# Kernel tuning notes

Hardware: AMD Instinct MI355X
Metric: run time of the kernel (lower is better)

Reference implementation:

```python
import jax, jax.numpy as jnp
import numpy as np

D_MODEL = 2048
N_HEADS = 16
N_KV_HEADS = 4
HEAD_DIM = D_MODEL // N_HEADS  # 128
N_REP = N_HEADS // N_KV_HEADS  # 4
WINDOW = 1024
NUM_META = 128
ROPE_BASE = 10000.0
EPS = 1e-6


def _rmsnorm(x, w):
    # x: [..., HEAD_DIM]; computed in fp32 like the torch module
    xf = x.astype(jnp.float32)
    rms = jax.lax.rsqrt(jnp.mean(xf * xf, axis=-1, keepdims=True) + EPS)
    return (w * xf * rms).astype(x.dtype)


def _apply_rope(x, pos):
    # x: [B, H, T, HEAD_DIM], pos: [B, T] (int) -> interleaved rotary
    inv_freq = 1.0 / (ROPE_BASE ** (jnp.arange(0, HEAD_DIM, 2, dtype=jnp.float32) / HEAD_DIM))  # [HEAD_DIM/2]
    freqs = pos.astype(jnp.float32)[..., None] * inv_freq  # [B, T, HEAD_DIM/2]
    cos = jnp.cos(freqs)[:, None, :, :]  # [B, 1, T, HEAD_DIM/2]
    sin = jnp.sin(freqs)[:, None, :, :]
    x1 = x[..., ::2]
    x2 = x[..., 1::2]
    rot = jnp.stack([x1 * cos - x2 * sin, x1 * sin + x2 * cos], axis=-1)  # [B,H,T,HEAD_DIM/2,2]
    return rot.reshape(x.shape)


def setup_inputs() -> dict:
    key = jax.random.key(0)
    kh, kq, kk, kv, ko = jax.random.split(key, 5)
    B, T = 2, 2048
    s = 0.02
    return {
        'hidden_states': jax.random.normal(kh, (B, T, D_MODEL), dtype=jnp.float32),
        'position_ids': jnp.arange(T, dtype=jnp.int32),
        'Wq': jax.random.normal(kq, (D_MODEL, N_HEADS * HEAD_DIM), dtype=jnp.float32) * s,
        'Wk': jax.random.normal(kk, (D_MODEL, N_KV_HEADS * HEAD_DIM), dtype=jnp.float32) * s,
        'Wv': jax.random.normal(kv, (D_MODEL, N_KV_HEADS * HEAD_DIM), dtype=jnp.float32) * s,
        'Wo': jax.random.normal(ko, (N_HEADS * HEAD_DIM, D_MODEL), dtype=jnp.float32) * s,
        'q_norm_w': jnp.ones((HEAD_DIM,), dtype=jnp.float32),
        'k_norm_w': jnp.ones((HEAD_DIM,), dtype=jnp.float32),
    }


def reference(hidden_states, position_ids, Wq, Wk, Wv, Wo, q_norm_w, k_norm_w):
    B, T, _ = hidden_states.shape
    Tk = T  # no kv_cache / shared_kv in this config

    # QKV projections -> [B, H, T, hd]
    q = (hidden_states @ Wq).reshape(B, T, N_HEADS, HEAD_DIM).transpose(0, 2, 1, 3)
    k = (hidden_states @ Wk).reshape(B, T, N_KV_HEADS, HEAD_DIM).transpose(0, 2, 1, 3)
    v = (hidden_states @ Wv).reshape(B, T, N_KV_HEADS, HEAD_DIM).transpose(0, 2, 1, 3)

    # per-head RMSNorm (before RoPE, as in the torch module)
    q = _rmsnorm(q, q_norm_w)
    k = _rmsnorm(k, k_norm_w)

    # RoPE: queries use position_ids, keys use arange(Tk)
    pos_q = jnp.broadcast_to(position_ids[None, :], (B, T))
    pos_k = jnp.broadcast_to(jnp.arange(Tk)[None, :], (B, Tk))
    q = _apply_rope(q, pos_q)
    k = _apply_rope(k, pos_k)

    # GQA: repeat KV heads (head h uses kv head h // N_REP)
    k = jnp.repeat(k, N_REP, axis=1)
    v = jnp.repeat(v, N_REP, axis=1)

    scale = 1.0 / np.sqrt(HEAD_DIM)
    scores = jnp.einsum('bhqd,bhkd->bhqk', q, k) * scale  # [B,H,T,Tk]

    # sliding-window + meta-token causal mask (offset = Tk - T = 0 here)
    q_idx = jnp.arange(T)[:, None]
    k_idx = jnp.arange(Tk)[None, :]
    win_start = jnp.maximum(q_idx - WINDOW + 1, NUM_META)
    allowed = (k_idx < NUM_META) | ((k_idx >= win_start) & (k_idx <= q_idx))
    scores = jnp.where(allowed[None, None], scores, -jnp.inf)

    probs = jax.nn.softmax(scores, axis=-1)
    out = jnp.einsum('bhqk,bhkd->bhqd', probs, v)  # [B,H,T,hd]
    out = out.transpose(0, 2, 1, 3).reshape(B, T, N_HEADS * HEAD_DIM)
    return out @ Wo
```

## Files before the change

kernel.cpp:

```cpp
#include <hip/hip_runtime.h>
#include <cstdint>
#include <cstddef>

#define DM 2048
#define TT 2048
#define BB 2
#define HQ 16
#define HKV 4
#define HD 128

typedef _Float16 f16;
using f16x8 = __attribute__((ext_vector_type(8))) f16;
using f32x4 = __attribute__((ext_vector_type(4))) float;
using f32x16 = __attribute__((ext_vector_type(16))) float;
using u32x4 = __attribute__((ext_vector_type(4))) uint32_t;

#define MFMA16(a, b, c) __builtin_amdgcn_mfma_f32_16x16x32_f16(a, b, c, 0, 0, 0)
#define MFMA32(a, b, c) __builtin_amdgcn_mfma_f32_32x32x16_f16(a, b, c, 0, 0, 0)

typedef __attribute__((address_space(1))) const void gvoid_t;
typedef __attribute__((address_space(3))) void lvoid_t;
static __device__ __forceinline__ void gload16(const void* g, void* l) {
  __builtin_amdgcn_global_load_lds((gvoid_t*)g, (lvoid_t*)l, 16, 0, 0);
}

static __device__ __forceinline__ float fast_exp2(float x) {
#if __has_builtin(__builtin_amdgcn_exp2f)
  return __builtin_amdgcn_exp2f(x);
#else
  return exp2f(x);
#endif
}

static __device__ __forceinline__ uint32_t cvt_pk_u32(float a, float b) {
  auto h2 = __builtin_amdgcn_cvt_pkrtz(a, b);
  return __builtin_bit_cast(uint32_t, h2);
}

__global__ __launch_bounds__(256) void k_cvt_f16(const float* __restrict__ in,
                                                 f16* __restrict__ out, int n8) {
  int i = blockIdx.x * 256 + threadIdx.x;
  if (i >= n8) return;
  const float4* pin = (const float4*)in;
  float4 a = pin[2 * i], b = pin[2 * i + 1];
  f16x8 o = {(f16)a.x, (f16)a.y, (f16)a.z, (f16)a.w,
             (f16)b.x, (f16)b.y, (f16)b.z, (f16)b.w};
  *(f16x8*)&out[(size_t)8 * i] = o;
}

__global__ __launch_bounds__(256) void k_tr_cvt(const float* __restrict__ in,
                                                f16* __restrict__ out, int N, int ldout) {
  __shared__ float tile[32][33];
  int n0 = blockIdx.x * 32, k0 = blockIdx.y * 32;
  int tx = threadIdx.x, ty = threadIdx.y;
#pragma unroll
  for (int r = 0; r < 32; r += 8) tile[ty + r][tx] = in[(size_t)(k0 + ty + r) * N + n0 + tx];
  __syncthreads();
#pragma unroll
  for (int r = 0; r < 32; r += 8)
    out[(size_t)(n0 + ty + r) * ldout + k0 + tx] = (f16)tile[tx][ty + r];
}

template <int BN_, int N_, bool OUT_F16>
__global__ __launch_bounds__(512, 2) void k_gemm8(const f16* __restrict__ A,
                                                  const f16* __restrict__ BT,
                                                  void* __restrict__ Cp, int M, int K) {
  constexpr int NF = BN_ / 64;
  constexpr int BI = BN_ / 64;
  __shared__ alignas(16) char Abuf[2][256 * 128];
  __shared__ alignas(16) char Bbuf[2][BN_ * 128];
  constexpr int NT = N_ / BN_;
  int bid = blockIdx.x;
  int m0 = (bid / NT) * 256, n0 = (bid % NT) * BN_;
  int tid = threadIdx.x;
  int lane = tid & 63, w = tid >> 6;
  int wr = w >> 2, wc = w & 3;
  int g = lane >> 4, c = lane & 15;
  int rswz = (c & 7) << 4;

  int srow = tid >> 3;
  int scbs = ((tid & 7) * 16) ^ ((srow & 7) << 4);
  const char* Ag = (const char*)A + (size_t)(m0 + srow) * (K * 2) + scbs;
  const char* Bg = (const char*)BT + (size_t)(n0 + srow) * (K * 2) + scbs;
  int lbase = w * 1024;

  f32x4 acc[8][NF] = {};
  int nk = K >> 6;

  auto stageA = [&](int buf, int kt, int i) {
    gload16(Ag + (size_t)(i * 64) * (K * 2) + (size_t)kt * 128,
            &Abuf[buf][i * 8192 + lbase]);
  };
  auto stageB = [&](int buf, int kt, int i) {
    gload16(Bg + (size_t)(i * 64) * (K * 2) + (size_t)kt * 128,
            &Bbuf[buf][i * 8192 + lbase]);
  };

  {
#pragma unroll
    for (int i = 0; i < 4; i++) stageA(0, 0, i);
#pragma unroll
    for (int i = 0; i < BI; i++) stageB(0, 0, i);
    asm volatile("s_waitcnt vmcnt(0)" ::: "memory");
    __builtin_amdgcn_s_barrier();
  }

  for (int kt = 0; kt < nk; kt++) {
    int cur = kt & 1, nxt = cur ^ 1;
    bool more = (kt + 1) < nk;
    const char* Ab = Abuf[cur];
    const char* Bb = Bbuf[cur];
    f16x8 bf[NF][2], af[2][2];
#pragma unroll
    for (int p = 0; p < 4; p++) {
      if (p == 0) {
#pragma unroll
        for (int nn = 0; nn < NF; nn++)
#pragma unroll
          for (int kk = 0; kk < 2; kk++) {
            int R = wc * (NF * 16) + nn * 16 + c;
            bf[nn][kk] = *(const f16x8*)(Bb + R * 128 + ((kk * 64 + g * 16) ^ rswz));
          }
      }
#pragma unroll
      for (int j = 0; j < 2; j++)
#pragma unroll
        for (int kk = 0; kk < 2; kk++) {
          int R = wr * 128 + (p * 2 + j) * 16 + c;
          af[j][kk] = *(const f16x8*)(Ab + R * 128 + ((kk * 64 + g * 16) ^ rswz));
        }
      if (more) {
        if (p == 0) {
          stageA(nxt, kt + 1, 0); stageA(nxt, kt + 1, 1); stageB(nxt, kt + 1, 0);
        } else if (p == 1) {
          stageA(nxt, kt + 1, 2); stageA(nxt, kt + 1, 3); stageB(nxt, kt + 1, 1);
          if constexpr (BI == 3) stageB(nxt, kt + 1, 2);
        }
      }
      __builtin_amdgcn_s_barrier();
      __builtin_amdgcn_s_setprio(1);
#pragma unroll
      for (int j = 0; j < 2; j++)
#pragma unroll
        for (int nn = 0; nn < NF; nn++)
#pragma unroll
          for (int kk = 0; kk < 2; kk++)
            acc[p * 2 + j][nn] = MFMA16(af[j][kk], bf[nn][kk], acc[p * 2 + j][nn]);
      __builtin_amdgcn_s_setprio(0);
    }
    asm volatile("s_waitcnt vmcnt(0)" ::: "memory");
    __builtin_amdgcn_s_barrier();
  }
#pragma unroll
  for (int mm = 0; mm < 8; mm++)
#pragma unroll
    for (int nn = 0; nn < NF; nn++)
#pragma unroll
      for (int r = 0; r < 4; r++) {
        size_t row = m0 + wr * 128 + mm * 16 + g * 4 + r;
        size_t col = n0 + wc * (NF * 16) + nn * 16 + c;
        float v = acc[mm][nn][r];
        if constexpr (OUT_F16)
          ((f16*)Cp)[row * N_ + col] = (f16)v;
        else
          ((float*)Cp)[row * N_ + col] = v;
      }
}

__global__ __launch_bounds__(256) void k_norm_rope(const f16* __restrict__ qkv,
                                                   const int* __restrict__ pos_ids,
                                                   const float* __restrict__ qw,
                                                   const float* __restrict__ kw,
                                                   f16* __restrict__ Qo, f16* __restrict__ Ko) {
  int bt = blockIdx.x;
  int b = bt >> 11, t = bt & 2047;
  int tid = threadIdx.x, w = tid >> 6, lane = tid & 63;
  const f16* row = qkv + (size_t)bt * 3072;
  float pq = (float)pos_ids[t];
  float pk = (float)t;
  float inv = expf(-(float)lane * 0.14391156831212787f);
  float aq = pq * inv, ak = pk * inv;
  float snq = sinf(aq), csq = cosf(aq);
  float snk = sinf(ak), csk = cosf(ak);
  for (int hi = w; hi < 20; hi += 4) {
    bool isq = hi < 16;
    int off = isq ? hi * 128 : 2048 + (hi - 16) * 128;
    float x1 = (float)row[off + 2 * lane];
    float x2 = (float)row[off + 2 * lane + 1];
    float ss = x1 * x1 + x2 * x2;
#pragma unroll
    for (int o = 1; o < 64; o <<= 1) ss += __shfl_xor(ss, o);
    float rms = rsqrtf(ss * (1.0f / 128.0f) + 1e-6f);
    const float* wt = isq ? qw : kw;
    float n1 = x1 * rms * wt[2 * lane], n2 = x2 * rms * wt[2 * lane + 1];
    float sn = isq ? snq : snk, cs = isq ? csq : csk;
    f16 r1 = (f16)(n1 * cs - n2 * sn), r2 = (f16)(n1 * sn + n2 * cs);
    if (isq) {
      f16* dst = Qo + (((size_t)b * HQ + hi) * TT + t) * HD;
      dst[2 * lane] = r1;
      dst[2 * lane + 1] = r2;
    } else {
      f16* dst = Ko + (((size_t)b * HKV + (hi - 16)) * TT + t) * HD;
      dst[2 * lane] = r1;
      dst[2 * lane + 1] = r2;
    }
  }
}

__global__ __launch_bounds__(256) void k_trV(const f16* __restrict__ qkv,
                                             f16* __restrict__ Vt) {
  __shared__ f16 tile[32][34];
  int t0 = blockIdx.x * 32, d0 = blockIdx.y * 32;
  int bh = blockIdx.z;
  int b = bh >> 2, hkv = bh & 3;
  int tx = threadIdx.x, ty = threadIdx.y;
  const f16* src = qkv + (size_t)b * 2048 * 3072 + 2560 + hkv * 128;
#pragma unroll
  for (int r = 0; r < 32; r += 8)
    tile[ty + r][tx] = src[(size_t)(t0 + ty + r) * 3072 + d0 + tx];
  __syncthreads();
  f16* dst = Vt + ((size_t)bh * HD + d0) * TT + t0;
#pragma unroll
  for (int r = 0; r < 32; r += 8)
    dst[(size_t)(ty + r) * TT + tx] = tile[tx][ty + r];
}

__global__ __launch_bounds__(256, 2) void k_attn2(const f16* __restrict__ Q,
                                                  const f16* __restrict__ Kc,
                                                  const f16* __restrict__ Vt,
                                                  f16* __restrict__ Oa) {
  __shared__ alignas(16) char KsC[2][64 * 256];
  __shared__ alignas(16) char VsC[2][128 * 128];
  int qt = blockIdx.x, h = blockIdx.y, b = blockIdx.z;
  qt = b ? (15 - qt) : qt;
  int q0 = qt * 128, hkv = h >> 2;
  int tid = threadIdx.x;
  int w = tid >> 6, lane = tid & 63, ln = lane & 31, hi = lane >> 5;
  const char* KbB = (const char*)(Kc + ((size_t)b * HKV + hkv) * TT * HD);
  const char* VbB = (const char*)(Vt + ((size_t)b * HKV + hkv) * (size_t)HD * TT);
  int q = q0 + w * 32 + ln;
  const f16* Qp = Q + (((size_t)b * HQ + h) * TT + q) * HD + hi * 8;
  f16x8 qf[8];
#pragma unroll
  for (int st = 0; st < 8; st++) qf[st] = *(const f16x8*)&Qp[st * 16];
  f32x16 o[4] = {};
  float lsum = 0.f;
  int kfswz = (ln & 7) << 4;

  int krow0 = w * 4 + (lane >> 4);
  int kswzb = ((lane & 15) * 16) ^ ((krow0 & 7) << 4);
  int vrow0 = w * 8 + (lane >> 3);
  int vswzb = ((lane & 7) * 16) ^ ((vrow0 & 7) << 4);

  int k0max = (q0 + 127) & ~63;
  int wlo = (q0 - 1023 > 128) ? ((q0 - 1023) & ~63) : 128;
  int nw = (k0max >= wlo) ? ((k0max - wlo) >> 6) + 1 : 0;
  int ntiles = 2 + nw;
  int qw = q0 + w * 32;

  const float C1 = 0.12751791217100872f;
  const float C2 = 5.7707801635534255f;

  auto stage = [&](int buf, int k0) {
    const char* ks = KbB + (size_t)(k0 + krow0) * 256 + kswzb;
    const char* vs = VbB + (size_t)vrow0 * (TT * 2) + (size_t)k0 * 2 + vswzb;
    char* kd = KsC[buf] + w * 1024;
    char* vd = VsC[buf] + w * 1024;
#pragma unroll
    for (int j = 0; j < 4; j++) gload16(ks + (size_t)j * 4096, kd + j * 4096);
#pragma unroll
    for (int j = 0; j < 4; j++) gload16(vs + (size_t)j * 32 * (TT * 2), vd + j * 4096);
  };

  stage(0, 0);
  __syncthreads();
  int cur = 0;

  for (int ti = 0; ti < ntiles; ti++) {
    int k0 = (ti < 2) ? ti * 64 : wlo + (ti - 2) * 64;
    bool havenext = (ti + 1 < ntiles);
    if (havenext) {
      int k0n = (ti + 1 < 2) ? 64 : wlo + (ti - 1) * 64;
      stage(cur ^ 1, k0n);
    }
    bool needmask = false;
    if (ti >= 2) {
      int wsmax = qw + 31 - 1023;
      if (wsmax < 128) wsmax = 128;
      needmask = !((k0 + 63 <= qw) && (k0 >= wsmax));
    }
    f16x8 pa[2][2];
#pragma unroll
    for (int ksub = 0; ksub < 2; ksub++) {
      f32x16 s0 = {}, s1 = {};
      const char* krow = KsC[cur] + (ksub * 32 + ln) * 256;
      __builtin_amdgcn_s_setprio(1);
#pragma unroll
      for (int st = 0; st < 8; st += 2) {
        f16x8 kf0 = *(const f16x8*)(krow + ((st * 32 + hi * 16) ^ kfswz));
        f16x8 kf1 = *(const f16x8*)(krow + (((st + 1) * 32 + hi * 16) ^ kfswz));
        s0 = MFMA32(kf0, qf[st], s0);
        s1 = MFMA32(kf1, qf[st + 1], s1);
      }
      __builtin_amdgcn_s_setprio(0);
      f32x16 s = s0 + s1;
      int qmk = q - (k0 + ksub * 32 + 4 * hi);
      float pr[16];
#pragma unroll
      for (int r = 0; r < 16; r++) {
        float e = fast_exp2(s[r] * C1 - C2);
        if (needmask) {
          int kk = (r & 3) + 8 * (r >> 2);
          e = ((uint32_t)(qmk - kk) < 1024u) ? e : 0.0f;
        }
        lsum += e;
        pr[r] = e;
      }
      uint32_t c[8];
#pragma unroll
      for (int i = 0; i < 8; i++) c[i] = cvt_pk_u32(pr[2 * i], pr[2 * i + 1]);
      {
        uint32_t x0 = __shfl_xor(c[0], 32), x1 = __shfl_xor(c[1], 32);
        uint32_t x2 = __shfl_xor(c[2], 32), x3 = __shfl_xor(c[3], 32);
        u32x4 t0 = {hi ? x2 : c[0], hi ? x3 : c[1], hi ? c[2] : x0, hi ? c[3] : x1};
        pa[ksub][0] = __builtin_bit_cast(f16x8, t0);
        uint32_t x4 = __shfl_xor(c[4], 32), x5 = __shfl_xor(c[5], 32);
        uint32_t x6 = __shfl_xor(c[6], 32), x7 = __shfl_xor(c[7], 32);
        u32x4 t1 = {hi ? x6 : c[4], hi ? x7 : c[5], hi ? c[6] : x4, hi ? c[7] : x5};
        pa[ksub][1] = __builtin_bit_cast(f16x8, t1);
      }
    }
    __builtin_amdgcn_s_setprio(1);
#pragma unroll
    for (int dsub = 0; dsub < 4; dsub++) {
      const char* vrow = VsC[cur] + (dsub * 32 + ln) * 128;
#pragma unroll
      for (int ksub = 0; ksub < 2; ksub++)
#pragma unroll
        for (int st2 = 0; st2 < 2; st2++) {
          f16x8 vf = *(const f16x8*)(vrow + ((ksub * 64 + st2 * 32 + hi * 16) ^ kfswz));
          o[dsub] = MFMA32(pa[ksub][st2], vf, o[dsub]);
        }
    }
    __builtin_amdgcn_s_setprio(0);
    __syncthreads();
    cur ^= 1;
  }
  lsum += __shfl_xor(lsum, 32);
  float rl[16];
#pragma unroll
  for (int r = 0; r < 16; r++) {
    int row = (r & 3) + 8 * (r >> 2) + 4 * hi;
    float lv = __shfl(lsum, row);
    rl[r] = 1.0f / lv;
  }
#pragma unroll
  for (int r = 0; r < 16; r++) {
    int row = (r & 3) + 8 * (r >> 2) + 4 * hi;
    size_t base = ((size_t)b * TT + q0 + w * 32 + row) * DM + (size_t)h * HD + ln;
#pragma unroll
    for (int dsub = 0; dsub < 4; dsub++)
      Oa[base + dsub * 32] = (f16)(o[dsub][r] * rl[r]);
  }
}

extern "C" void kernel_launch(void* const* d_in, const int* in_sizes, int n_in,
                              void* d_out, int out_size, void* d_ws, size_t ws_size,
                              hipStream_t stream) {
  const float* hidden = (const float*)d_in[0];
  const int* pos = (const int*)d_in[1];
  const float* Wq = (const float*)d_in[2];
  const float* Wk = (const float*)d_in[3];
  const float* Wv = (const float*)d_in[4];
  const float* Wo = (const float*)d_in[5];
  const float* qw = (const float*)d_in[6];
  const float* kw = (const float*)d_in[7];
  float* out = (float*)d_out;

  char* p = (char*)d_ws;
  auto take = [&](size_t n) {
    void* r = (void*)p;
    p += (n + 255) & ~(size_t)255;
    return r;
  };
  f16* Xb = (f16*)take((size_t)4096 * 2048 * 2);
  f16* WqkvT = (f16*)take((size_t)3072 * 2048 * 2);
  f16* WoT = (f16*)take((size_t)2048 * 2048 * 2);
  f16* QKVb = (f16*)take((size_t)4096 * 3072 * 2);
  f16* Qr = (f16*)take((size_t)BB * HQ * TT * HD * 2);
  f16* Kr = (f16*)take((size_t)BB * HKV * TT * HD * 2);
  f16* Vt = (f16*)take((size_t)BB * HKV * TT * HD * 2);
  f16* Attn = (f16*)take((size_t)4096 * 2048 * 2);

  dim3 tb(32, 8);
  k_cvt_f16<<<4096, 256, 0, stream>>>(hidden, Xb, 1048576);
  k_tr_cvt<<<dim3(64, 64), tb, 0, stream>>>(Wq, WqkvT, 2048, 2048);
  k_tr_cvt<<<dim3(16, 64), tb, 0, stream>>>(Wk, WqkvT + (size_t)2048 * 2048, 512, 2048);
  k_tr_cvt<<<dim3(16, 64), tb, 0, stream>>>(Wv, WqkvT + (size_t)2560 * 2048, 512, 2048);
  k_tr_cvt<<<dim3(64, 64), tb, 0, stream>>>(Wo, WoT, 2048, 2048);
  k_gemm8<192, 3072, true><<<256, 512, 0, stream>>>(Xb, WqkvT, QKVb, 4096, 2048);
  k_norm_rope<<<4096, 256, 0, stream>>>(QKVb, pos, qw, kw, Qr, Kr);
  k_trV<<<dim3(64, 4, 8), tb, 0, stream>>>(QKVb, Vt);
  k_attn2<<<dim3(16, 16, 2), 256, 0, stream>>>(Qr, Kr, Vt, Attn);
  k_gemm8<128, 2048, false><<<256, 512, 0, stream>>>(Attn, WoT, out, 4096, 2048);
}
```

Baseline: 199.9 us.

## Merge weight transposes into one launch, remap GEMM blocks and attention q-tiles

Combines the four weight transpose/convert launches into a single kernel that dispatches on block index, cutting launch overhead and the tail gaps between launches. The GEMM block index is permuted with a stride-8 remap, probably to spread tiles sharing A/B rows across XCDs or L2 for better cache locality. Attention q-tile ordering now interleaves short and long causal tiles within each batch, to balance load across concurrently scheduled blocks. Each remap changes which CUs get which work and could lower cache reuse if the assumed block scheduling does not hold.

```diff
diff --git a/kernel.cpp b/kernel.cpp
--- a/kernel.cpp
+++ b/kernel.cpp
@@ -48,17 +48,34 @@
   *(f16x8*)&out[(size_t)8 * i] = o;
 }
 
-__global__ __launch_bounds__(256) void k_tr_cvt(const float* __restrict__ in,
-                                                f16* __restrict__ out, int N, int ldout) {
+__global__ __launch_bounds__(256) void k_tr_all(const float* __restrict__ Wq,
+                                                const float* __restrict__ Wk,
+                                                const float* __restrict__ Wv,
+                                                const float* __restrict__ Wo,
+                                                f16* __restrict__ WqkvT,
+                                                f16* __restrict__ WoT) {
   __shared__ float tile[32][33];
-  int n0 = blockIdx.x * 32, k0 = blockIdx.y * 32;
+  int t = blockIdx.x;
+  const float* in;
+  f16* out;
+  int N, nx;
+  if (t < 4096) {
+    in = Wq; out = WqkvT; N = 2048; nx = 64;
+  } else if (t < 5120) {
+    t -= 4096; in = Wk; out = WqkvT + (size_t)2048 * 2048; N = 512; nx = 16;
+  } else if (t < 6144) {
+    t -= 5120; in = Wv; out = WqkvT + (size_t)2560 * 2048; N = 512; nx = 16;
+  } else {
+    t -= 6144; in = Wo; out = WoT; N = 2048; nx = 64;
+  }
+  int n0 = (t % nx) * 32, k0 = (t / nx) * 32;
   int tx = threadIdx.x, ty = threadIdx.y;
 #pragma unroll
   for (int r = 0; r < 32; r += 8) tile[ty + r][tx] = in[(size_t)(k0 + ty + r) * N + n0 + tx];
   __syncthreads();
 #pragma unroll
   for (int r = 0; r < 32; r += 8)
-    out[(size_t)(n0 + ty + r) * ldout + k0 + tx] = (f16)tile[tx][ty + r];
+    out[(size_t)(n0 + ty + r) * 2048 + k0 + tx] = (f16)tile[tx][ty + r];
 }
 
 template <int BN_, int N_, bool OUT_F16>
@@ -70,7 +87,8 @@
   __shared__ alignas(16) char Abuf[2][256 * 128];
   __shared__ alignas(16) char Bbuf[2][BN_ * 128];
   constexpr int NT = N_ / BN_;
-  int bid = blockIdx.x;
+  int bid0 = blockIdx.x;
+  int bid = (bid0 & 7) * (gridDim.x >> 3) + (bid0 >> 3);
   int m0 = (bid / NT) * 256, n0 = (bid % NT) * BN_;
   int tid = threadIdx.x;
   int lane = tid & 63, w = tid >> 6;
@@ -232,7 +250,7 @@
   __shared__ alignas(16) char KsC[2][64 * 256];
   __shared__ alignas(16) char VsC[2][128 * 128];
   int qt = blockIdx.x, h = blockIdx.y, b = blockIdx.z;
-  qt = b ? (15 - qt) : qt;
+  qt = (qt & 1) ? (15 - (qt >> 1)) : (qt >> 1);
   int q0 = qt * 128, hkv = h >> 2;
   int tid = threadIdx.x;
   int w = tid >> 6, lane = tid & 63, ln = lane & 31, hi = lane >> 5;
@@ -394,10 +412,7 @@
 
   dim3 tb(32, 8);
   k_cvt_f16<<<4096, 256, 0, stream>>>(hidden, Xb, 1048576);
-  k_tr_cvt<<<dim3(64, 64), tb, 0, stream>>>(Wq, WqkvT, 2048, 2048);
-  k_tr_cvt<<<dim3(16, 64), tb, 0, stream>>>(Wk, WqkvT + (size_t)2048 * 2048, 512, 2048);
-  k_tr_cvt<<<dim3(16, 64), tb, 0, stream>>>(Wv, WqkvT + (size_t)2560 * 2048, 512, 2048);
-  k_tr_cvt<<<dim3(64, 64), tb, 0, stream>>>(Wo, WoT, 2048, 2048);
+  k_tr_all<<<10240, tb, 0, stream>>>(Wq, Wk, Wv, Wo, WqkvT, WoT);
   k_gemm8<192, 3072, true><<<256, 512, 0, stream>>>(Xb, WqkvT, QKVb, 4096, 2048);
   k_norm_rope<<<4096, 256, 0, stream>>>(QKVb, pos, qw, kw, Qr, Kr);
   k_trV<<<dim3(64, 4, 8), tb, 0, stream>>>(QKVb, Vt);
```

After: 197.8 us. No clear change (-1.1%).
